# Kernel tuning notes

Measured on AMD Instinct MI355X. Metric: run time of the kernel, lower is better.

The kernel has to match this reference:

```python
import jax, jax.numpy as jnp
import numpy as np

B, C, H, W, K = 8, 256, 128, 128, 9
P = K // 2
DN = ('NCHW', 'OIHW', 'NCHW')


def _dw(x, w, pad):
    # depthwise conv: w has shape (C,1,kh,kw), feature_group_count=C
    return jax.lax.conv_general_dilated(
        x, w, window_strides=(1, 1), padding=pad,
        dimension_numbers=DN, feature_group_count=C)


def setup_inputs() -> dict:
    key = jax.random.key(0)
    ks = jax.random.split(key, 6)
    s = 1.0 / np.sqrt(K)
    return {
        'x': jax.random.normal(ks[0], (B, C, H, W), dtype=jnp.float32),
        'wh1': jax.random.normal(ks[1], (C, 1, 1, K), dtype=jnp.float32) * s,
        'wh2': jax.random.normal(ks[2], (C, 1, 1, K), dtype=jnp.float32) * s,
        'wv1': jax.random.normal(ks[3], (C, 1, K, 1), dtype=jnp.float32) * s,
        'wv2': jax.random.normal(ks[4], (C, 1, K, 1), dtype=jnp.float32) * s,
        'wproj': jax.random.normal(ks[5], (C, 4 * C), dtype=jnp.float32) / np.sqrt(4 * C),
    }


def reference(x, wh1, wh2, wv1, wv2, wproj):
    pad_h = ((0, 0), (P, P))  # 1xK conv pads width
    pad_v = ((P, P), (0, 0))  # Kx1 conv pads height
    y = jnp.concatenate([
        _dw(x, wh1, pad_h),
        _dw(x, wh2, pad_h),
        _dw(x, wv1, pad_v),
        _dw(x, wv2, pad_v),
    ], axis=1)  # (B, 4C, H, W)
    out = jnp.einsum('oc,bchw->bohw', wproj, y)  # 1x1 projection
    return jax.nn.relu(out)
```

## Files before the change

### kernel.cpp

```cpp
#include <hip/hip_runtime.h>
#include <hip/hip_bf16.h>

#define BB 8
#define CC 256
#define HH 128
#define WW 128
#define KS 9
#define PADR 4
#define NPIX (BB*HH*WW)
#define KDIM (4*CC)

typedef __attribute__((ext_vector_type(8))) short bf16x8;
typedef __attribute__((ext_vector_type(4))) float f32x4;

static __device__ __forceinline__ unsigned short f2bf(float f) {
  union { float f; unsigned u; } v; v.f = f;
  unsigned r = v.u + 0x7FFF + ((v.u >> 16) & 1);
  return (unsigned short)(r >> 16);
}

static __device__ __forceinline__ void gload_lds16(const void* g, void* l) {
  __builtin_amdgcn_global_load_lds(
      (const __attribute__((address_space(1))) void*)g,
      (__attribute__((address_space(3))) void*)l, 16, 0, 0);
}

__global__ void prep_kernel(const float* __restrict__ wproj,
                            unsigned short* __restrict__ Ap) {
  int idx = blockIdx.x * 256 + threadIdx.x;
  int o  = idx >> 10;
  int kp = idx & 1023;
  int c  = kp >> 2;
  int t  = kp & 3;
  Ap[idx] = f2bf(wproj[o * 1024 + t * 256 + c]);
}

__global__ __launch_bounds__(256)
void conv_kernel(const float* __restrict__ x,
                 const float* __restrict__ wh1, const float* __restrict__ wh2,
                 const float* __restrict__ wv1, const float* __restrict__ wv2,
                 unsigned short* __restrict__ Y) {
  int bid = blockIdx.x;
  bid = (bid & 7) * 128 + (bid >> 3);
  int h = bid & 127;
  int c = threadIdx.x;

  float W1[KS], W2[KS], W3[KS], W4[KS];
#pragma unroll
  for (int k = 0; k < KS; ++k) {
    W1[k] = wh1[c * KS + k];
    W2[k] = wh2[c * KS + k];
    W3[k] = wv1[c * KS + k];
    W4[k] = wv2[c * KS + k];
  }

  int b = bid >> 7;
  const float* xc = x + ((size_t)(b * CC + c)) * (HH * WW);
  unsigned short* yrow = Y + (size_t)bid * 128 * KDIM + (size_t)c * 4;

  for (int w0 = 0; w0 < WW; w0 += 8) {
    float hw[16];
    {
      const float* xr = xc + h * WW;
#pragma unroll
      for (int s = 0; s < 4; ++s) {
        int wb = w0 - 4 + s * 4;
        float4 seg;
        if (wb >= 0 && wb <= WW - 4) seg = *(const float4*)(xr + wb);
        else seg = make_float4(0.f, 0.f, 0.f, 0.f);
        hw[s*4+0]=seg.x; hw[s*4+1]=seg.y; hw[s*4+2]=seg.z; hw[s*4+3]=seg.w;
      }
    }
    float vv[KS][8];
#pragma unroll
    for (int k = 0; k < KS; ++k) {
      int r = h + k - PADR;
      if (r >= 0 && r < HH) {
        const float* rp = xc + r * WW + w0;
        float4 a = *(const float4*)(rp);
        float4 b4 = *(const float4*)(rp + 4);
        vv[k][0]=a.x; vv[k][1]=a.y; vv[k][2]=a.z; vv[k][3]=a.w;
        vv[k][4]=b4.x; vv[k][5]=b4.y; vv[k][6]=b4.z; vv[k][7]=b4.w;
      } else {
#pragma unroll
        for (int j = 0; j < 8; ++j) vv[k][j] = 0.f;
      }
    }
#pragma unroll
    for (int w = 0; w < 8; ++w) {
      float s1 = 0.f, s2 = 0.f, s3 = 0.f, s4 = 0.f;
#pragma unroll
      for (int k = 0; k < KS; ++k) {
        float xh = hw[w + k];
        s1 = fmaf(xh, W1[k], s1);
        s2 = fmaf(xh, W2[k], s2);
        float xv = vv[k][w];
        s3 = fmaf(xv, W3[k], s3);
        s4 = fmaf(xv, W4[k], s4);
      }
      unsigned u0 = (unsigned)f2bf(s1) | ((unsigned)f2bf(s2) << 16);
      unsigned u1 = (unsigned)f2bf(s3) | ((unsigned)f2bf(s4) << 16);
      *(uint2*)(yrow + (size_t)(w0 + w) * KDIM) = make_uint2(u0, u1);
    }
  }
}

__global__ __launch_bounds__(256)
void gemm_kernel(const unsigned short* __restrict__ Ap,
                 const unsigned short* __restrict__ Yg,
                 float* __restrict__ out) {
  __shared__ short As[128 * 64];
  __shared__ short Bs[128 * 64];

  int bid = blockIdx.x;
  bid = (bid & 7) * 256 + (bid >> 3);
  int otile = bid & 1;
  int pt    = bid >> 1;
  int tid   = threadIdx.x;
  int lane  = tid & 63;
  int wv    = tid >> 6;
  int om    = wv & 1;
  int pn    = wv >> 1;
  int l15   = lane & 15;
  int kseg  = lane >> 4;

  const short* A  = (const short*)Ap + (size_t)(otile * 128) * KDIM;
  const short* Bg = (const short*)Yg + (size_t)pt * 128 * KDIM;

  int srow = tid >> 3;
  int skc  = (tid & 7) * 8;

  f32x4 acc[4][4] = {};

  for (int k0 = 0; k0 < KDIM; k0 += 64) {
#pragma unroll
    for (int i = 0; i < 4; ++i) {
      int rr = i * 32 + srow;
      gload_lds16(A  + (size_t)rr * KDIM + k0 + skc, &As[rr * 64 + skc]);
      gload_lds16(Bg + (size_t)rr * KDIM + k0 + skc, &Bs[rr * 64 + skc]);
    }
    __syncthreads();
#pragma unroll
    for (int kk = 0; kk < 2; ++kk) {
      bf16x8 af[4], bfr[4];
#pragma unroll
      for (int m = 0; m < 4; ++m)
        af[m] = *(const bf16x8*)&As[(om * 64 + m * 16 + l15) * 64 + kk * 32 + kseg * 8];
#pragma unroll
      for (int n = 0; n < 4; ++n)
        bfr[n] = *(const bf16x8*)&Bs[(pn * 64 + n * 16 + l15) * 64 + kk * 32 + kseg * 8];
#pragma unroll
      for (int m = 0; m < 4; ++m)
#pragma unroll
        for (int n = 0; n < 4; ++n)
          acc[m][n] = __builtin_amdgcn_mfma_f32_16x16x32_bf16(af[m], bfr[n],
                                                              acc[m][n], 0, 0, 0);
    }
    __syncthreads();
  }

  int b = pt >> 7, h = pt & 127;
#pragma unroll
  for (int m = 0; m < 4; ++m) {
#pragma unroll
    for (int n = 0; n < 4; ++n) {
#pragma unroll
      for (int r = 0; r < 4; ++r) {
        int o = otile * 128 + om * 64 + m * 16 + kseg * 4 + r;
        int w = pn * 64 + n * 16 + l15;
        out[((size_t)(b * 256 + o) << 14) + (h << 7) + w] =
            fmaxf(acc[m][n][r], 0.f);
      }
    }
  }
}

extern "C" void kernel_launch(void* const* d_in, const int* in_sizes, int n_in,
                              void* d_out, int out_size, void* d_ws, size_t ws_size,
                              hipStream_t stream) {
  (void)in_sizes; (void)n_in; (void)out_size; (void)ws_size;
  const float* x     = (const float*)d_in[0];
  const float* wh1   = (const float*)d_in[1];
  const float* wh2   = (const float*)d_in[2];
  const float* wv1   = (const float*)d_in[3];
  const float* wv2   = (const float*)d_in[4];
  const float* wproj = (const float*)d_in[5];
  float* out = (float*)d_out;

  unsigned short* Yg = (unsigned short*)d_ws;
  unsigned short* Ap = (unsigned short*)((char*)d_ws
                        + (size_t)NPIX * KDIM * sizeof(unsigned short));

  hipLaunchKernelGGL(prep_kernel, dim3(KDIM * CC / 256), dim3(256), 0, stream,
                     wproj, Ap);
  hipLaunchKernelGGL(conv_kernel, dim3(BB * HH), dim3(256), 0, stream,
                     x, wh1, wh2, wv1, wv2, Yg);
  hipLaunchKernelGGL(gemm_kernel, dim3(2 * BB * HH), dim3(512 / 2), 0, stream,
                     Ap, Yg, out);
}
```

Before: 553.8 us.

## Transpose input to channels-last bf16, restructure conv as sliding window, widen GEMM tile

```diff
diff --git a/kernel.cpp b/kernel.cpp
--- a/kernel.cpp
+++ b/kernel.cpp
@@ -6,7 +6,6 @@
 #define HH 128
 #define WW 128
 #define KS 9
-#define PADR 4
 #define NPIX (BB*HH*WW)
 #define KDIM (4*CC)
 
@@ -17,6 +16,10 @@
   union { float f; unsigned u; } v; v.f = f;
   unsigned r = v.u + 0x7FFF + ((v.u >> 16) & 1);
   return (unsigned short)(r >> 16);
+}
+static __device__ __forceinline__ float bf2f(unsigned short u) {
+  union { unsigned u; float f; } v; v.u = ((unsigned)u) << 16;
+  return v.f;
 }
 
 static __device__ __forceinline__ void gload_lds16(const void* g, void* l) {
@@ -35,96 +38,136 @@
   Ap[idx] = f2bf(wproj[o * 1024 + t * 256 + c]);
 }
 
+__global__ void wprep_kernel(const float* __restrict__ wh1,
+                             const float* __restrict__ wh2,
+                             const float* __restrict__ wv1,
+                             const float* __restrict__ wv2,
+                             float* __restrict__ wt) {
+  int idx = blockIdx.x * 256 + threadIdx.x;
+  int c = idx & 255;
+  int q = idx >> 8;
+  int cv = q / 9, k = q % 9;
+  const float* src = (cv == 0) ? wh1 : (cv == 1) ? wh2 : (cv == 2) ? wv1 : wv2;
+  wt[idx] = src[c * KS + k];
+}
+
 __global__ __launch_bounds__(256)
-void conv_kernel(const float* __restrict__ x,
-                 const float* __restrict__ wh1, const float* __restrict__ wh2,
-                 const float* __restrict__ wv1, const float* __restrict__ wv2,
+void transpose_kernel(const float* __restrict__ x,
+                      unsigned short* __restrict__ xt) {
+  __shared__ float lds[64][65];
+  int g   = blockIdx.x;
+  int b   = g >> 10;
+  int r   = g & 1023;
+  int ct  = r >> 8;
+  int hwt = r & 255;
+  int c0  = ct * 64, hw0 = hwt * 64;
+  const float* in = x + (size_t)b * CC * (HH * WW);
+  unsigned short* outp = xt + (size_t)b * (HH * WW) * CC;
+
+  int tr  = threadIdx.x >> 4;
+  int tc4 = (threadIdx.x & 15) * 4;
+
+#pragma unroll
+  for (int s = 0; s < 4; ++s) {
+    int row = tr + s * 16;
+    float4 v = *(const float4*)(in + (size_t)(c0 + row) * (HH * WW) + hw0 + tc4);
+    lds[row][tc4 + 0] = v.x; lds[row][tc4 + 1] = v.y;
+    lds[row][tc4 + 2] = v.z; lds[row][tc4 + 3] = v.w;
+  }
+  __syncthreads();
+#pragma unroll
+  for (int s = 0; s < 4; ++s) {
+    int row_o = tr + s * 16;
+    ushort4 o;
+    o.x = f2bf(lds[tc4 + 0][row_o]);
+    o.y = f2bf(lds[tc4 + 1][row_o]);
+    o.z = f2bf(lds[tc4 + 2][row_o]);
+    o.w = f2bf(lds[tc4 + 3][row_o]);
+    *(ushort4*)(outp + (size_t)(hw0 + row_o) * CC + c0 + tc4) = o;
+  }
+}
+
+__global__ __launch_bounds__(256)
+void conv_kernel(const unsigned short* __restrict__ xt,
+                 const float* __restrict__ wt,
                  unsigned short* __restrict__ Y) {
-  int bid = blockIdx.x;
-  bid = (bid & 7) * 128 + (bid >> 3);
-  int h = bid & 127;
-  int c = threadIdx.x;
+  int g  = blockIdx.x;
+  int sb = (g & 7) * 512 + (g >> 3);
+  int w  = sb & 127;
+  int tq = sb >> 7;
+  int hs = tq & 3;
+  int b  = tq >> 2;
+  int c  = threadIdx.x;
 
   float W1[KS], W2[KS], W3[KS], W4[KS];
 #pragma unroll
   for (int k = 0; k < KS; ++k) {
-    W1[k] = wh1[c * KS + k];
-    W2[k] = wh2[c * KS + k];
-    W3[k] = wv1[c * KS + k];
-    W4[k] = wv2[c * KS + k];
-  }
-
-  int b = bid >> 7;
-  const float* xc = x + ((size_t)(b * CC + c)) * (HH * WW);
-  unsigned short* yrow = Y + (size_t)bid * 128 * KDIM + (size_t)c * 4;
-
-  for (int w0 = 0; w0 < WW; w0 += 8) {
-    float hw[16];
-    {
-      const float* xr = xc + h * WW;
-#pragma unroll
-      for (int s = 0; s < 4; ++s) {
-        int wb = w0 - 4 + s * 4;
-        float4 seg;
-        if (wb >= 0 && wb <= WW - 4) seg = *(const float4*)(xr + wb);
-        else seg = make_float4(0.f, 0.f, 0.f, 0.f);
-        hw[s*4+0]=seg.x; hw[s*4+1]=seg.y; hw[s*4+2]=seg.z; hw[s*4+3]=seg.w;
-      }
-    }
-    float vv[KS][8];
+    W1[k] = wt[(0 * KS + k) * CC + c];
+    W2[k] = wt[(1 * KS + k) * CC + c];
+    W3[k] = wt[(2 * KS + k) * CC + c];
+    W4[k] = wt[(3 * KS + k) * CC + c];
+  }
+
+  const unsigned short* xb = xt + (size_t)b * (HH * WW) * CC;
+  int h0 = hs * 32;
+
+  float vwin[9];
+#pragma unroll
+  for (int i = 0; i < 8; ++i) {
+    int row = h0 - 4 + i;
+    vwin[i] = (row >= 0) ? bf2f(xb[(size_t)(row * WW + w) * CC + c]) : 0.f;
+  }
+
+#pragma unroll
+  for (int s = 0; s < 32; ++s) {
+    int h  = h0 + s;
+    int rv = h + 4;
+    vwin[8] = (rv < HH) ? bf2f(xb[(size_t)(rv * WW + w) * CC + c]) : 0.f;
+
+    float hwin[9];
+#pragma unroll
+    for (int j = 0; j < 9; ++j) {
+      if (j == 4) { hwin[j] = vwin[4]; continue; }
+      int wp = w - 4 + j;
+      hwin[j] = (wp >= 0 && wp < WW) ? bf2f(xb[(size_t)(h * WW + wp) * CC + c]) : 0.f;
+    }
+
+    float s1 = 0.f, s2 = 0.f, s3 = 0.f, s4 = 0.f;
 #pragma unroll
     for (int k = 0; k < KS; ++k) {
-      int r = h + k - PADR;
-      if (r >= 0 && r < HH) {
-        const float* rp = xc + r * WW + w0;
-        float4 a = *(const float4*)(rp);
-        float4 b4 = *(const float4*)(rp + 4);
-        vv[k][0]=a.x; vv[k][1]=a.y; vv[k][2]=a.z; vv[k][3]=a.w;
-        vv[k][4]=b4.x; vv[k][5]=b4.y; vv[k][6]=b4.z; vv[k][7]=b4.w;
-      } else {
-#pragma unroll
-        for (int j = 0; j < 8; ++j) vv[k][j] = 0.f;
-      }
-    }
-#pragma unroll
-    for (int w = 0; w < 8; ++w) {
-      float s1 = 0.f, s2 = 0.f, s3 = 0.f, s4 = 0.f;
-#pragma unroll
-      for (int k = 0; k < KS; ++k) {
-        float xh = hw[w + k];
-        s1 = fmaf(xh, W1[k], s1);
-        s2 = fmaf(xh, W2[k], s2);
-        float xv = vv[k][w];
-        s3 = fmaf(xv, W3[k], s3);
-        s4 = fmaf(xv, W4[k], s4);
-      }
-      unsigned u0 = (unsigned)f2bf(s1) | ((unsigned)f2bf(s2) << 16);
-      unsigned u1 = (unsigned)f2bf(s3) | ((unsigned)f2bf(s4) << 16);
-      *(uint2*)(yrow + (size_t)(w0 + w) * KDIM) = make_uint2(u0, u1);
-    }
-  }
-}
-
-__global__ __launch_bounds__(256)
+      s1 = fmaf(hwin[k], W1[k], s1);
+      s2 = fmaf(hwin[k], W2[k], s2);
+      s3 = fmaf(vwin[k], W3[k], s3);
+      s4 = fmaf(vwin[k], W4[k], s4);
+    }
+    unsigned u0 = (unsigned)f2bf(s1) | ((unsigned)f2bf(s2) << 16);
+    unsigned u1 = (unsigned)f2bf(s3) | ((unsigned)f2bf(s4) << 16);
+    size_t p = (size_t)(b * (HH * WW) + h * WW + w);
+    *(uint2*)(Y + p * KDIM + c * 4) = make_uint2(u0, u1);
+
+#pragma unroll
+    for (int i = 0; i < 8; ++i) vwin[i] = vwin[i + 1];
+  }
+}
+
+__global__ __launch_bounds__(512)
 void gemm_kernel(const unsigned short* __restrict__ Ap,
                  const unsigned short* __restrict__ Yg,
                  float* __restrict__ out) {
-  __shared__ short As[128 * 64];
+  __shared__ short As[256 * 64];
   __shared__ short Bs[128 * 64];
 
   int bid = blockIdx.x;
-  bid = (bid & 7) * 256 + (bid >> 3);
-  int otile = bid & 1;
-  int pt    = bid >> 1;
-  int tid   = threadIdx.x;
-  int lane  = tid & 63;
-  int wv    = tid >> 6;
-  int om    = wv & 1;
-  int pn    = wv >> 1;
-  int l15   = lane & 15;
-  int kseg  = lane >> 4;
-
-  const short* A  = (const short*)Ap + (size_t)(otile * 128) * KDIM;
+  int pt  = (bid & 7) * 128 + (bid >> 3);
+  int tid  = threadIdx.x;
+  int lane = tid & 63;
+  int wv   = tid >> 6;
+  int om   = wv & 3;
+  int pn   = wv >> 2;
+  int l15  = lane & 15;
+  int kseg = lane >> 4;
+
+  const short* A  = (const short*)Ap;
   const short* Bg = (const short*)Yg + (size_t)pt * 128 * KDIM;
 
   int srow = tid >> 3;
@@ -135,8 +178,12 @@
   for (int k0 = 0; k0 < KDIM; k0 += 64) {
 #pragma unroll
     for (int i = 0; i < 4; ++i) {
-      int rr = i * 32 + srow;
-      gload_lds16(A  + (size_t)rr * KDIM + k0 + skc, &As[rr * 64 + skc]);
+      int rr = i * 64 + srow;
+      gload_lds16(A + (size_t)rr * KDIM + k0 + skc, &As[rr * 64 + skc]);
+    }
+#pragma unroll
+    for (int i = 0; i < 2; ++i) {
+      int rr = i * 64 + srow;
       gload_lds16(Bg + (size_t)rr * KDIM + k0 + skc, &Bs[rr * 64 + skc]);
     }
     __syncthreads();
@@ -166,7 +213,7 @@
     for (int n = 0; n < 4; ++n) {
 #pragma unroll
       for (int r = 0; r < 4; ++r) {
-        int o = otile * 128 + om * 64 + m * 16 + kseg * 4 + r;
+        int o = om * 64 + m * 16 + kseg * 4 + r;
         int w = pn * 64 + n * 16 + l15;
         out[((size_t)(b * 256 + o) << 14) + (h << 7) + w] =
             fmaxf(acc[m][n][r], 0.f);
@@ -187,14 +234,18 @@
   const float* wproj = (const float*)d_in[5];
   float* out = (float*)d_out;
 
-  unsigned short* Yg = (unsigned short*)d_ws;
-  unsigned short* Ap = (unsigned short*)((char*)d_ws
-                        + (size_t)NPIX * KDIM * sizeof(unsigned short));
-
-  hipLaunchKernelGGL(prep_kernel, dim3(KDIM * CC / 256), dim3(256), 0, stream,
-                     wproj, Ap);
-  hipLaunchKernelGGL(conv_kernel, dim3(BB * HH), dim3(256), 0, stream,
-                     x, wh1, wh2, wv1, wv2, Yg);
-  hipLaunchKernelGGL(gemm_kernel, dim3(2 * BB * HH), dim3(512 / 2), 0, stream,
-                     Ap, Yg, out);
-}
+  char* wsb = (char*)d_ws;
+  unsigned short* Yg = (unsigned short*)wsb;
+  unsigned short* Xt = (unsigned short*)(wsb + (size_t)NPIX * KDIM * 2);
+  unsigned short* Ap = (unsigned short*)(wsb + (size_t)NPIX * KDIM * 2
+                                             + (size_t)NPIX * CC * 2);
+  float* Wt = (float*)(wsb + (size_t)NPIX * KDIM * 2
+                           + (size_t)NPIX * CC * 2 + (size_t)CC * KDIM * 2);
+
+  hipLaunchKernelGGL(prep_kernel, dim3(1024), dim3(256), 0, stream, wproj, Ap);
+  hipLaunchKernelGGL(wprep_kernel, dim3(36), dim3(256), 0, stream,
+                     wh1, wh2, wv1, wv2, Wt);
+  hipLaunchKernelGGL(transpose_kernel, dim3(8192), dim3(256), 0, stream, x, Xt);
+  hipLaunchKernelGGL(conv_kernel, dim3(4096), dim3(256), 0, stream, Xt, Wt, Yg);
+  hipLaunchKernelGGL(gemm_kernel, dim3(1024), dim3(512), 0, stream, Ap, Yg, out);
+}
```

Result: slower. 605.6 us (+9.4%).
